# Optimization experiments

Hardware: AMD Instinct MI355X
Metric: run time of the kernel (lower is better)

## Reference

```python
import jax, jax.numpy as jnp
import numpy as np

NUM_HEADS = 4
SCALE = 0.17677669529663687  # head_dim(32) ** -0.5


def setup_inputs() -> dict:
    key = jax.random.key(0)
    k1, k2 = jax.random.split(key)
    qkv = jax.random.normal(k1, (1024, 144, 384), dtype=jnp.float32)
    mask = jax.random.normal(k2, (1, 4, 144, 144), dtype=jnp.float32)
    return {"qkv": qkv, "mask": mask}


def reference(qkv, mask):
    B, N, C = qkv.shape
    hd = C // NUM_HEADS // 3  # head_dim = 32
    # [B,N,3,H,hd] -> [3,B,H,N,hd]
    qkv = qkv.reshape(B, N, 3, NUM_HEADS, hd).transpose(2, 0, 3, 1, 4)
    q, k, v = qkv[0] * SCALE, qkv[1], qkv[2]
    attn = jnp.einsum("bhqd,bhkd->bhqk", q, k) + mask  # mask broadcasts over B
    attn = jax.nn.softmax(attn, axis=-1)
    out = jnp.einsum("bhqk,bhkd->bhqd", attn, v)  # [B,H,N,hd]
    return out.transpose(0, 2, 1, 3).reshape(B, N, C // 3)
```

## Files before the change

### kernel.cpp

```cpp
#include <hip/hip_runtime.h>
#include <hip/hip_bf16.h>
#include <stdint.h>

#define NB 1024
#define NN 144
#define NH 4
#define HDIM 32
#define CC 384
#define SCALE_F 0.17677669529663687f

#define KSTR 40
#define VSTR 168
#define PSTR 168

typedef __attribute__((ext_vector_type(8))) short short8;
typedef __attribute__((ext_vector_type(4))) float float4v;

__device__ __forceinline__ uint16_t f2b(float f) {
    __hip_bfloat16 h = __float2bfloat16(f);
    return *reinterpret_cast<uint16_t*>(&h);
}

__global__ __launch_bounds__(192, 3) void attn_kernel(
    const float* __restrict__ qkv,
    const float* __restrict__ mask,
    float* __restrict__ out)
{
    __shared__ __align__(16) uint16_t Kl[NN * KSTR];
    __shared__ __align__(16) uint16_t Vt[HDIM * VSTR];
    __shared__ __align__(16) uint16_t Pb[3 * 16 * PSTR];

    const int bid  = blockIdx.x;
    const int b    = ((bid >> 5) << 3) | (bid & 7);
    const int h    = (bid >> 3) & 3;
    const int tid  = threadIdx.x;
    const int wave = tid >> 6;
    const int lane = tid & 63;
    const int col  = lane & 15;
    const int quad = lane >> 4;

    const float* qkv_b = qkv + (size_t)b * (NN * CC);
    const float* mbase = mask + h * (NN * NN);

    float4 kbuf[6], vbuf[6];
    #pragma unroll
    for (int i = 0; i < 6; i++) {
        const int idx = tid + i * 192;
        const int ki = idx >> 3;
        const int g  = idx & 7;
        kbuf[i] = *(const float4*)(qkv_b + ki * CC + 128 + h * HDIM + g * 4);
        vbuf[i] = *(const float4*)(qkv_b + ki * CC + 256 + h * HDIM + g * 4);
    }

    float4 qbuf[3][2];
    #pragma unroll
    for (int s3 = 0; s3 < 3; s3++) {
        const int qi0 = (wave + s3 * 3) * 16;
        const float* qp = qkv_b + (size_t)(qi0 + col) * CC + h * HDIM + quad * 8;
        qbuf[s3][0] = ((const float4*)qp)[0];
        qbuf[s3][1] = ((const float4*)qp)[1];
    }

    float4 mreg[9];
    {
        const int qi0 = wave * 16;
        #pragma unroll
        for (int t = 0; t < 9; t++)
            mreg[t] = *(const float4*)&mbase[(qi0 + col) * NN + t * 16 + quad * 4];
    }

    #pragma unroll
    for (int i = 0; i < 6; i++) {
        const int idx = tid + i * 192;
        const int ki = idx >> 3;
        const int g  = idx & 7;
        ushort4 kp;
        kp.x = f2b(kbuf[i].x); kp.y = f2b(kbuf[i].y);
        kp.z = f2b(kbuf[i].z); kp.w = f2b(kbuf[i].w);
        *(ushort4*)&Kl[ki * KSTR + g * 4] = kp;

        const int d0 = g * 4;
        Vt[(d0 + 0) * VSTR + ki] = f2b(vbuf[i].x);
        Vt[(d0 + 1) * VSTR + ki] = f2b(vbuf[i].y);
        Vt[(d0 + 2) * VSTR + ki] = f2b(vbuf[i].z);
        Vt[(d0 + 3) * VSTR + ki] = f2b(vbuf[i].w);
    }
    for (int i = tid; i < HDIM * 16; i += 192)
        Vt[(i >> 4) * VSTR + NN + (i & 15)] = 0;
    uint16_t* Pw = &Pb[wave * 16 * PSTR];
    for (int i = lane; i < 16 * 16; i += 64)
        Pw[(i >> 4) * PSTR + NN + (i & 15)] = 0;

    __syncthreads();

    const float4v zf = {0.f, 0.f, 0.f, 0.f};

    short8 ones;
    #pragma unroll
    for (int j = 0; j < 8; j++) ones[j] = (short)0x3F80;

    #pragma unroll
    for (int s3 = 0; s3 < 3; s3++) {
        const int qi0 = (wave + s3 * 3) * 16;

        short8 qfrag;
        qfrag[0] = (short)f2b(qbuf[s3][0].x); qfrag[1] = (short)f2b(qbuf[s3][0].y);
        qfrag[2] = (short)f2b(qbuf[s3][0].z); qfrag[3] = (short)f2b(qbuf[s3][0].w);
        qfrag[4] = (short)f2b(qbuf[s3][1].x); qfrag[5] = (short)f2b(qbuf[s3][1].y);
        qfrag[6] = (short)f2b(qbuf[s3][1].z); qfrag[7] = (short)f2b(qbuf[s3][1].w);

        float4v S[9];
        #pragma unroll
        for (int t = 0; t < 9; t++) {
            short8 kfrag = *(const short8*)&Kl[(t * 16 + col) * KSTR + quad * 8];
            S[t] = __builtin_amdgcn_mfma_f32_16x16x32_bf16(kfrag, qfrag, zf, 0, 0, 0);
        }

        #pragma unroll
        for (int t = 0; t < 9; t++) {
            ushort4 pp;
            pp.x = f2b(__expf(fmaf(S[t][0], SCALE_F, mreg[t].x)));
            pp.y = f2b(__expf(fmaf(S[t][1], SCALE_F, mreg[t].y)));
            pp.z = f2b(__expf(fmaf(S[t][2], SCALE_F, mreg[t].z)));
            pp.w = f2b(__expf(fmaf(S[t][3], SCALE_F, mreg[t].w)));
            *(ushort4*)&Pw[col * PSTR + t * 16 + quad * 4] = pp;
        }

        if (s3 < 2) {
            const int qn = (wave + (s3 + 1) * 3) * 16;
            #pragma unroll
            for (int t = 0; t < 9; t++)
                mreg[t] = *(const float4*)&mbase[(qn + col) * NN + t * 16 + quad * 4];
        }

        float4v O0 = zf, O1 = zf, L = zf;
        #pragma unroll
        for (int kt = 0; kt < 5; kt++) {
            short8 pfrag = *(const short8*)&Pw[col * PSTR + kt * 32 + quad * 8];
            short8 vf0   = *(const short8*)&Vt[col * VSTR + kt * 32 + quad * 8];
            short8 vf1   = *(const short8*)&Vt[(16 + col) * VSTR + kt * 32 + quad * 8];
            O0 = __builtin_amdgcn_mfma_f32_16x16x32_bf16(pfrag, vf0, O0, 0, 0, 0);
            O1 = __builtin_amdgcn_mfma_f32_16x16x32_bf16(pfrag, vf1, O1, 0, 0, 0);
            L  = __builtin_amdgcn_mfma_f32_16x16x32_bf16(pfrag, ones, L, 0, 0, 0);
        }

        float* ob = out + ((size_t)b * NN + qi0) * 128 + h * HDIM;
        #pragma unroll
        for (int r = 0; r < 4; r++) {
            float inv = 1.0f / L[r];
            int orow = (quad * 4 + r) * 128;
            ob[orow + col]      = O0[r] * inv;
            ob[orow + 16 + col] = O1[r] * inv;
        }
    }
}

extern "C" void kernel_launch(void* const* d_in, const int* in_sizes, int n_in,
                              void* d_out, int out_size, void* d_ws, size_t ws_size,
                              hipStream_t stream) {
    const float* qkv  = (const float*)d_in[0];
    const float* mask = (const float*)d_in[1];
    float* out        = (float*)d_out;
    attn_kernel<<<dim3(NB * NH), dim3(192), 0, stream>>>(qkv, mask, out);
}
```

Before: 338.9 us.

## Keep softmax probabilities in registers via permlane swaps instead of LDS staging

Removes the per-wave LDS buffer for the bf16 probability matrix. The MFMA output layout is remapped into the A-operand layout for the PV MFMA using v_permlane32_swap and v_permlane16_swap across packed bf16 pairs. This drops the LDS writes and reads and cuts shared memory, and launch bounds rise to 4 blocks per SM to use that. It relies on the permlane swap instructions being present on gfx950 and on the lane remapping matching the k-ordering that V expects.

```diff
diff --git a/kernel.cpp b/kernel.cpp
--- a/kernel.cpp
+++ b/kernel.cpp
@@ -11,24 +11,40 @@
 
 #define KSTR 40
 #define VSTR 168
-#define PSTR 168
 
 typedef __attribute__((ext_vector_type(8))) short short8;
 typedef __attribute__((ext_vector_type(4))) float float4v;
+typedef __attribute__((ext_vector_type(4))) unsigned int uint4v;
 
 __device__ __forceinline__ uint16_t f2b(float f) {
     __hip_bfloat16 h = __float2bfloat16(f);
     return *reinterpret_cast<uint16_t*>(&h);
 }
 
-__global__ __launch_bounds__(192, 3) void attn_kernel(
+__device__ __forceinline__ void plswap32(uint32_t& x, uint32_t& y) {
+#if __has_builtin(__builtin_amdgcn_permlane32_swap)
+    auto r = __builtin_amdgcn_permlane32_swap(x, y, false, false);
+    x = r[0]; y = r[1];
+#else
+    asm volatile("v_permlane32_swap_b32 %0, %1" : "+v"(x), "+v"(y));
+#endif
+}
+__device__ __forceinline__ void plswap16(uint32_t& x, uint32_t& y) {
+#if __has_builtin(__builtin_amdgcn_permlane16_swap)
+    auto r = __builtin_amdgcn_permlane16_swap(x, y, false, false);
+    x = r[0]; y = r[1];
+#else
+    asm volatile("v_permlane16_swap_b32 %0, %1" : "+v"(x), "+v"(y));
+#endif
+}
+
+__global__ __launch_bounds__(192, 4) void attn_kernel(
     const float* __restrict__ qkv,
     const float* __restrict__ mask,
     float* __restrict__ out)
 {
     __shared__ __align__(16) uint16_t Kl[NN * KSTR];
     __shared__ __align__(16) uint16_t Vt[HDIM * VSTR];
-    __shared__ __align__(16) uint16_t Pb[3 * 16 * PSTR];
 
     const int bid  = blockIdx.x;
     const int b    = ((bid >> 5) << 3) | (bid & 7);
@@ -61,14 +77,6 @@
         qbuf[s3][1] = ((const float4*)qp)[1];
     }
 
-    float4 mreg[9];
-    {
-        const int qi0 = wave * 16;
-        #pragma unroll
-        for (int t = 0; t < 9; t++)
-            mreg[t] = *(const float4*)&mbase[(qi0 + col) * NN + t * 16 + quad * 4];
-    }
-
     #pragma unroll
     for (int i = 0; i < 6; i++) {
         const int idx = tid + i * 192;
@@ -87,9 +95,14 @@
     }
     for (int i = tid; i < HDIM * 16; i += 192)
         Vt[(i >> 4) * VSTR + NN + (i & 15)] = 0;
-    uint16_t* Pw = &Pb[wave * 16 * PSTR];
-    for (int i = lane; i < 16 * 16; i += 64)
-        Pw[(i >> 4) * PSTR + NN + (i & 15)] = 0;
+
+    float4 mreg[9];
+    {
+        const int qi0 = wave * 16;
+        #pragma unroll
+        for (int t = 0; t < 9; t++)
+            mreg[t] = *(const float4*)&mbase[(qi0 + col) * NN + t * 16 + quad * 4];
+    }
 
     __syncthreads();
 
@@ -116,14 +129,15 @@
             S[t] = __builtin_amdgcn_mfma_f32_16x16x32_bf16(kfrag, qfrag, zf, 0, 0, 0);
         }
 
+        uint32_t pd[9][2];
         #pragma unroll
         for (int t = 0; t < 9; t++) {
-            ushort4 pp;
-            pp.x = f2b(__expf(fmaf(S[t][0], SCALE_F, mreg[t].x)));
-            pp.y = f2b(__expf(fmaf(S[t][1], SCALE_F, mreg[t].y)));
-            pp.z = f2b(__expf(fmaf(S[t][2], SCALE_F, mreg[t].z)));
-            pp.w = f2b(__expf(fmaf(S[t][3], SCALE_F, mreg[t].w)));
-            *(ushort4*)&Pw[col * PSTR + t * 16 + quad * 4] = pp;
+            uint32_t e0 = f2b(__expf(fmaf(S[t][0], SCALE_F, mreg[t].x)));
+            uint32_t e1 = f2b(__expf(fmaf(S[t][1], SCALE_F, mreg[t].y)));
+            uint32_t e2 = f2b(__expf(fmaf(S[t][2], SCALE_F, mreg[t].z)));
+            uint32_t e3 = f2b(__expf(fmaf(S[t][3], SCALE_F, mreg[t].w)));
+            pd[t][0] = e0 | (e1 << 16);
+            pd[t][1] = e2 | (e3 << 16);
         }
 
         if (s3 < 2) {
@@ -136,9 +150,21 @@
         float4v O0 = zf, O1 = zf, L = zf;
         #pragma unroll
         for (int kt = 0; kt < 5; kt++) {
-            short8 pfrag = *(const short8*)&Pw[col * PSTR + kt * 32 + quad * 8];
-            short8 vf0   = *(const short8*)&Vt[col * VSTR + kt * 32 + quad * 8];
-            short8 vf1   = *(const short8*)&Vt[(16 + col) * VSTR + kt * 32 + quad * 8];
+            const int t0 = 2 * kt, t1 = 2 * kt + 1;
+            uint32_t d0 = pd[t0][0];
+            uint32_t d1 = pd[t0][1];
+            uint32_t d2 = (t1 < 9) ? pd[t1][0] : 0u;
+            uint32_t d3 = (t1 < 9) ? pd[t1][1] : 0u;
+            plswap32(d0, d2);
+            plswap32(d1, d3);
+            plswap16(d0, d2);
+            plswap16(d1, d3);
+            uint4v dw;
+            dw.x = d0; dw.y = d1; dw.z = d2; dw.w = d3;
+            short8 pfrag = __builtin_bit_cast(short8, dw);
+
+            short8 vf0 = *(const short8*)&Vt[col * VSTR + kt * 32 + quad * 8];
+            short8 vf1 = *(const short8*)&Vt[(16 + col) * VSTR + kt * 32 + quad * 8];
             O0 = __builtin_amdgcn_mfma_f32_16x16x32_bf16(pfrag, vf0, O0, 0, 0, 0);
             O1 = __builtin_amdgcn_mfma_f32_16x16x32_bf16(pfrag, vf1, O1, 0, 0, 0);
             L  = __builtin_amdgcn_mfma_f32_16x16x32_bf16(pfrag, ones, L, 0, 0, 0);
```

New measurement: 338.0 us. No clear change (-0.3%).
